# Kernel optimization log

Hardware: AMD Instinct MI355X
Metric: run time of the kernel (lower is better)

## Reference

```python
import jax, jax.numpy as jnp
import numpy as np

N_NODES = 50000
N_EDGES = 1500000
D = 512
LN_EPS = 1e-5


def setup_inputs() -> dict:
    key = jax.random.key(0)
    ks = jax.random.split(key, 8)
    scale = 1.0 / np.sqrt(D)
    return {
        "node_feature": jax.random.normal(ks[0], (N_NODES, D), dtype=jnp.float32),
        "edge_index": jax.random.randint(ks[1], (2, N_EDGES), 0, N_NODES, dtype=jnp.int32),
        "W_l": jax.random.uniform(ks[2], (D, D), jnp.float32, -scale, scale),  # neighbor lin
        "b_l": jnp.zeros((D,), jnp.float32),
        "W_r": jax.random.uniform(ks[3], (D, D), jnp.float32, -scale, scale),  # root lin (no bias)
        "gamma": jnp.ones((D,), jnp.float32),
        "beta": jnp.zeros((D,), jnp.float32),
    }


def _layer_norm(x, gamma, beta):
    mu = jnp.mean(x, axis=-1, keepdims=True)
    var = jnp.mean(jnp.square(x - mu), axis=-1, keepdims=True)
    return (x - mu) * jax.lax.rsqrt(var + LN_EPS) * gamma + beta


def reference(node_feature, edge_index, W_l, b_l, W_r, gamma, beta):
    n = node_feature.shape[0]
    residual = node_feature
    h = _layer_norm(node_feature, gamma, beta)
    src, dst = edge_index[0], edge_index[1]
    # mean-aggregate source features at destinations (gather + segment scatter)
    summed = jax.ops.segment_sum(h[src], dst, num_segments=n)  # [N, D]
    cnt = jax.ops.segment_sum(jnp.ones((src.shape[0],), h.dtype), dst, num_segments=n)
    mean = summed / jnp.maximum(cnt, 1.0)[:, None]
    # SAGEConv: lin_l(aggregated) + lin_r(root); bias on lin_l
    out = mean @ W_l.T + b_l + h @ W_r.T
    out = jax.nn.relu(out)
    return out + residual
```

## Files before the change

### kernel.cpp

```cpp
#include <hip/hip_runtime.h>


#define D_DIM 512

typedef __bf16 bf16x8 __attribute__((ext_vector_type(8)));
typedef float f32x4 __attribute__((ext_vector_type(4)));
typedef float f32x2 __attribute__((ext_vector_type(2)));

__device__ __forceinline__ unsigned short f2bf(float f) {
  unsigned u = __float_as_uint(f);
  u += 0x7fffu + ((u >> 16) & 1u);
  return (unsigned short)(u >> 16);
}
__device__ __forceinline__ float bflo(unsigned u) { return __uint_as_float(u << 16); }
__device__ __forceinline__ float bfhi(unsigned u) { return __uint_as_float(u & 0xffff0000u); }
__device__ __forceinline__ unsigned packbf2(float lo, float hi) {
  return (unsigned)f2bf(lo) | ((unsigned)f2bf(hi) << 16);
}

__global__ void ln_kernel(const float* __restrict__ x, const float* __restrict__ gamma,
                          const float* __restrict__ beta, unsigned short* __restrict__ Acat,
                          unsigned char* __restrict__ h8, int n, int use_fp8) {
  int lane = threadIdx.x & 63;
  int row = blockIdx.x * 4 + (threadIdx.x >> 6);
  if (row >= n) return;
  const float* xr = x + (size_t)row * D_DIM + lane * 8;
  float4 a = *(const float4*)xr;
  float4 b = *(const float4*)(xr + 4);
  float sum = a.x + a.y + a.z + a.w + b.x + b.y + b.z + b.w;
  float sq = a.x * a.x + a.y * a.y + a.z * a.z + a.w * a.w +
             b.x * b.x + b.y * b.y + b.z * b.z + b.w * b.w;
#pragma unroll
  for (int m = 1; m < 64; m <<= 1) {
    sum += __shfl_xor(sum, m, 64);
    sq  += __shfl_xor(sq, m, 64);
  }
  float mu = sum * (1.0f / D_DIM);
  float var = sq * (1.0f / D_DIM) - mu * mu;
  float rs = rsqrtf(var + 1e-5f);
  const float* gp = gamma + lane * 8;
  const float* bp = beta + lane * 8;
  float4 g0 = *(const float4*)gp, g1 = *(const float4*)(gp + 4);
  float4 e0 = *(const float4*)bp, e1 = *(const float4*)(bp + 4);
  float h0 = (a.x - mu) * rs * g0.x + e0.x;
  float h1 = (a.y - mu) * rs * g0.y + e0.y;
  float h2 = (a.z - mu) * rs * g0.z + e0.z;
  float h3 = (a.w - mu) * rs * g0.w + e0.w;
  float h4 = (b.x - mu) * rs * g1.x + e1.x;
  float h5 = (b.y - mu) * rs * g1.y + e1.y;
  float h6 = (b.z - mu) * rs * g1.z + e1.z;
  float h7 = (b.w - mu) * rs * g1.w + e1.w;
  uint4 st = { packbf2(h0, h1), packbf2(h2, h3), packbf2(h4, h5), packbf2(h6, h7) };
  *(uint4*)(Acat + (size_t)row * 1024 + 512 + lane * 8) = st;
  if (use_fp8) {
    int p0 = __builtin_amdgcn_cvt_pk_fp8_f32(h0, h1, 0, false);
    p0 = __builtin_amdgcn_cvt_pk_fp8_f32(h2, h3, p0, true);
    int p1 = __builtin_amdgcn_cvt_pk_fp8_f32(h4, h5, 0, false);
    p1 = __builtin_amdgcn_cvt_pk_fp8_f32(h6, h7, p1, true);
    uint2 st2 = { (unsigned)p0, (unsigned)p1 };
    *(uint2*)(h8 + (size_t)row * 512 + lane * 8) = st2;
  }
}

__global__ void wconv_kernel(const float* __restrict__ Wl, const float* __restrict__ Wr,
                             unsigned short* __restrict__ Wcat) {
  int id = blockIdx.x * 256 + threadIdx.x;
  int j = id >> 9, k = id & 511;
  Wcat[(size_t)j * 1024 + k] = f2bf(Wl[id]);
  Wcat[(size_t)j * 1024 + 512 + k] = f2bf(Wr[id]);
}

__global__ void zero_kernel(int* __restrict__ p, int n) {
  int i = blockIdx.x * 256 + threadIdx.x;
  if (i < n) p[i] = 0;
}

__global__ void hist_kernel(const int* __restrict__ dst, int nE, int* __restrict__ cnt) {
  int e = blockIdx.x * 256 + threadIdx.x;
  if (e < nE) atomicAdd(&cnt[dst[e]], 1);
}

__global__ void scan1_kernel(const int* __restrict__ cnt, int n,
                             int* __restrict__ excl, int* __restrict__ bsums) {
  __shared__ int wsum[16];
  int gid = blockIdx.x * 1024 + threadIdx.x;
  int lane = threadIdx.x & 63, wave = threadIdx.x >> 6;
  int v = (gid < n) ? cnt[gid] : 0;
  int s = v;
#pragma unroll
  for (int d = 1; d < 64; d <<= 1) {
    int t = __shfl_up(s, d, 64);
    if (lane >= d) s += t;
  }
  if (lane == 63) wsum[wave] = s;
  __syncthreads();
  if (wave == 0) {
    int ws = (lane < 16) ? wsum[lane] : 0;
#pragma unroll
    for (int d = 1; d < 16; d <<= 1) {
      int t = __shfl_up(ws, d, 64);
      if (lane >= d) ws += t;
    }
    if (lane < 16) wsum[lane] = ws;
  }
  __syncthreads();
  int incl = s + ((wave > 0) ? wsum[wave - 1] : 0);
  if (gid < n) excl[gid] = incl - v;
  if (threadIdx.x == 1023) bsums[blockIdx.x] = incl;
}

__global__ void scan2_kernel(int* __restrict__ bsums, int nb) {
  int lane = threadIdx.x;
  int v = (lane < nb) ? bsums[lane] : 0;
  int s = v;
#pragma unroll
  for (int d = 1; d < 64; d <<= 1) {
    int t = __shfl_up(s, d, 64);
    if (lane >= d) s += t;
  }
  if (lane < nb) bsums[lane] = s - v;
}

__global__ void scan3_kernel(int* __restrict__ rowst, int* __restrict__ cur,
                             const int* __restrict__ bsums, int n, int nE) {
  int gid = blockIdx.x * 1024 + threadIdx.x;
  if (gid < n) {
    int r = rowst[gid] + bsums[blockIdx.x];
    rowst[gid] = r;
    cur[gid] = r;
  }
  if (gid == 0) rowst[n] = nE;
}

__global__ void scatter_kernel(const int* __restrict__ src, const int* __restrict__ dst,
                               int nE, int* __restrict__ cur, int* __restrict__ sorted_src) {
  int e = blockIdx.x * 256 + threadIdx.x;
  if (e < nE) {
    int p = atomicAdd(&cur[dst[e]], 1);
    sorted_src[p] = src[e];
  }
}

__device__ __forceinline__ void acc_bf(float* acc, uint4 r) {
  acc[0] += bflo(r.x); acc[1] += bfhi(r.x);
  acc[2] += bflo(r.y); acc[3] += bfhi(r.y);
  acc[4] += bflo(r.z); acc[5] += bfhi(r.z);
  acc[6] += bflo(r.w); acc[7] += bfhi(r.w);
}

__device__ __forceinline__ void acc_f8(float* acc, uint2 r) {
  f32x2 a = __builtin_amdgcn_cvt_pk_f32_fp8(r.x, false);
  f32x2 b = __builtin_amdgcn_cvt_pk_f32_fp8(r.x, true);
  f32x2 c = __builtin_amdgcn_cvt_pk_f32_fp8(r.y, false);
  f32x2 d = __builtin_amdgcn_cvt_pk_f32_fp8(r.y, true);
  acc[0] += a.x; acc[1] += a.y; acc[2] += b.x; acc[3] += b.y;
  acc[4] += c.x; acc[5] += c.y; acc[6] += d.x; acc[7] += d.y;
}

__global__ void agg_kernel(unsigned short* __restrict__ Acat,
                           const unsigned char* __restrict__ h8,
                           const int* __restrict__ rowst,
                           const int* __restrict__ sorted_src, int n, int use_fp8) {
  int lane = threadIdx.x & 63;
  int node = blockIdx.x * 4 + (threadIdx.x >> 6);
  if (node >= n) return;
  int s0 = rowst[node], s1 = rowst[node + 1];
  float acc[8] = {0.f, 0.f, 0.f, 0.f, 0.f, 0.f, 0.f, 0.f};
  if (use_fp8) {
    const unsigned char* hb = h8 + lane * 8;
    int e = s0;
    for (; e + 3 < s1; e += 4) {
      int i0 = sorted_src[e], i1 = sorted_src[e + 1];
      int i2 = sorted_src[e + 2], i3 = sorted_src[e + 3];
      uint2 r0 = *(const uint2*)(hb + (size_t)i0 * 512);
      uint2 r1 = *(const uint2*)(hb + (size_t)i1 * 512);
      uint2 r2 = *(const uint2*)(hb + (size_t)i2 * 512);
      uint2 r3 = *(const uint2*)(hb + (size_t)i3 * 512);
      acc_f8(acc, r0); acc_f8(acc, r1); acc_f8(acc, r2); acc_f8(acc, r3);
    }
    for (; e < s1; ++e) {
      uint2 r0 = *(const uint2*)(hb + (size_t)sorted_src[e] * 512);
      acc_f8(acc, r0);
    }
  } else {
    const unsigned short* hbase = Acat + 512 + lane * 8;
    int e = s0;
    for (; e + 3 < s1; e += 4) {
      int i0 = sorted_src[e], i1 = sorted_src[e + 1];
      int i2 = sorted_src[e + 2], i3 = sorted_src[e + 3];
      uint4 r0 = *(const uint4*)(hbase + (size_t)i0 * 1024);
      uint4 r1 = *(const uint4*)(hbase + (size_t)i1 * 1024);
      uint4 r2 = *(const uint4*)(hbase + (size_t)i2 * 1024);
      uint4 r3 = *(const uint4*)(hbase + (size_t)i3 * 1024);
      acc_bf(acc, r0); acc_bf(acc, r1); acc_bf(acc, r2); acc_bf(acc, r3);
    }
    for (; e < s1; ++e) {
      uint4 r0 = *(const uint4*)(hbase + (size_t)sorted_src[e] * 1024);
      acc_bf(acc, r0);
    }
  }
  int deg = s1 - s0;
  float sc = (deg > 0) ? (1.0f / (float)deg) : 0.0f;
  uint4 st = { packbf2(acc[0] * sc, acc[1] * sc), packbf2(acc[2] * sc, acc[3] * sc),
               packbf2(acc[4] * sc, acc[5] * sc), packbf2(acc[6] * sc, acc[7] * sc) };
  *(uint4*)(Acat + (size_t)node * 1024 + lane * 8) = st;
}

__device__ __forceinline__ void async16(const unsigned short* g, char* lds) {
  __builtin_amdgcn_global_load_lds((const __attribute__((address_space(1))) void*)g,
                                   (__attribute__((address_space(3))) void*)lds, 16, 0, 0);
}

__global__ __launch_bounds__(256) void gemm_kernel(
    const unsigned short* __restrict__ A,
    const unsigned short* __restrict__ B,
    const float* __restrict__ bias,
    const float* __restrict__ residual,
    float* __restrict__ out, int M, int Mblocks) {
  __shared__ unsigned short sA[2][4096];
  __shared__ unsigned short sB[2][4096];
  const int K = 1024;
  int t = threadIdx.x;
  int lane = t & 63, wave = t >> 6;
  int quad = lane >> 4, l16 = lane & 15;
  int b = blockIdx.x;
  int mb = (b >> 5) * 8 + (b & 7);
  int nb = (b >> 3) & 3;
  if (mb >= Mblocks) return;
  int mBase = mb * 128, nBase = nb * 128;
  int wm = (wave & 1) * 64, wn = (wave >> 1) * 64;

  const unsigned short* gA = A + (size_t)(mBase + (t >> 2)) * K + (t & 3) * 8;
  const unsigned short* gB = B + (size_t)(nBase + (t >> 2)) * K + (t & 3) * 8;

  f32x4 acc[4][4] = {};

  auto issue = [&](int ks, int buf) {
    char* a0 = (char*)&sA[buf][0] + wave * 1024;
    char* b0 = (char*)&sB[buf][0] + wave * 1024;
    async16(gA + ks, a0);
    async16(gA + (size_t)64 * K + ks, a0 + 4096);
    async16(gB + ks, b0);
    async16(gB + (size_t)64 * K + ks, b0 + 4096);
  };
  auto compute = [&](int buf) {
    const unsigned short* pA = &sA[buf][0];
    const unsigned short* pB = &sB[buf][0];
    bf16x8 af[4], bfr[4];
#pragma unroll
    for (int i = 0; i < 4; ++i)
      af[i] = *(const bf16x8*)(pA + (wm + i * 16 + l16) * 32 + quad * 8);
#pragma unroll
    for (int j = 0; j < 4; ++j)
      bfr[j] = *(const bf16x8*)(pB + (wn + j * 16 + l16) * 32 + quad * 8);
#pragma unroll
    for (int i = 0; i < 4; ++i)
#pragma unroll
      for (int j = 0; j < 4; ++j)
        acc[i][j] = __builtin_amdgcn_mfma_f32_16x16x32_bf16(af[i], bfr[j], acc[i][j], 0, 0, 0);
  };

  issue(0, 0);
  for (int r = 0; r < 31; ++r) {
    int cur = r & 1;
    issue((r + 1) << 5, cur ^ 1);
    asm volatile("s_waitcnt vmcnt(4)\n\ts_barrier" ::: "memory");
    compute(cur);
    asm volatile("s_barrier" ::: "memory");
  }
  asm volatile("s_waitcnt vmcnt(0)\n\ts_barrier" ::: "memory");
  compute(1);

  float biasv[4];
#pragma unroll
  for (int j = 0; j < 4; ++j) biasv[j] = bias[nBase + wn + j * 16 + l16];
#pragma unroll
  for (int i = 0; i < 4; ++i) {
    int gr0 = mBase + wm + i * 16 + quad * 4;
#pragma unroll
    for (int j = 0; j < 4; ++j) {
      int col = nBase + wn + j * 16 + l16;
#pragma unroll
      for (int r = 0; r < 4; ++r) {
        int gr = gr0 + r;
        if (gr < M) {
          size_t idx = (size_t)gr * D_DIM + col;
          float v = acc[i][j][r] + biasv[j];
          float rv = __builtin_nontemporal_load(&residual[idx]);
          __builtin_nontemporal_store(fmaxf(v, 0.0f) + rv, &out[idx]);
        }
      }
    }
  }
}

extern "C" void kernel_launch(void* const* d_in, const int* in_sizes, int n_in,
                              void* d_out, int out_size, void* d_ws, size_t ws_size,
                              hipStream_t stream) {
  const float* x = (const float*)d_in[0];
  const int* ei = (const int*)d_in[1];
  const float* Wl = (const float*)d_in[2];
  const float* bl = (const float*)d_in[3];
  const float* Wr = (const float*)d_in[4];
  const float* gamma = (const float*)d_in[5];
  const float* beta = (const float*)d_in[6];
  float* out = (float*)d_out;

  int n = in_sizes[0] / D_DIM;
  int nE = in_sizes[1] / 2;
  const int* src = ei;
  const int* dstv = ei + nE;
  int Mpad = (n + 127) & ~127;
  int Mblocks = Mpad / 128;

  char* w = (char*)d_ws;
  size_t off = 0;
  auto carve = [&](size_t bytes) {
    char* p = w + off;
    off += (bytes + 255) & ~(size_t)255;
    return p;
  };
  unsigned short* Acat = (unsigned short*)carve((size_t)Mpad * 1024 * 2);
  unsigned short* Wcat = (unsigned short*)carve((size_t)512 * 1024 * 2);
  int* sorted = (int*)carve((size_t)nE * 4);
  int* cnt = (int*)carve((size_t)n * 4);
  int* rowst = (int*)carve((size_t)(n + 1) * 4);
  int* bsums = (int*)carve(1024);
  if (off > ws_size) return;

  size_t h8_bytes = (size_t)n * 512;
  int use_fp8 = (off + h8_bytes <= ws_size) ? 1 : 0;
  unsigned char* h8 = use_fp8 ? (unsigned char*)carve(h8_bytes) : (unsigned char*)w;

  int nbScan = (n + 1023) / 1024;

  ln_kernel<<<(n + 3) / 4, 256, 0, stream>>>(x, gamma, beta, Acat, h8, n, use_fp8);
  wconv_kernel<<<(512 * 512) / 256, 256, 0, stream>>>(Wl, Wr, Wcat);
  zero_kernel<<<(n + 255) / 256, 256, 0, stream>>>(cnt, n);
  hist_kernel<<<(nE + 255) / 256, 256, 0, stream>>>(dstv, nE, cnt);
  scan1_kernel<<<nbScan, 1024, 0, stream>>>(cnt, n, rowst, bsums);
  scan2_kernel<<<1, 64, 0, stream>>>(bsums, nbScan);
  scan3_kernel<<<nbScan, 1024, 0, stream>>>(rowst, cnt, bsums, n, nE);
  scatter_kernel<<<(nE + 255) / 256, 256, 0, stream>>>(src, dstv, nE, cnt, sorted);
  agg_kernel<<<(n + 3) / 4, 256, 0, stream>>>(Acat, h8, rowst, sorted, n, use_fp8);
  int gemmBlocks = ((Mblocks + 7) / 8) * 32;
  gemm_kernel<<<gemmBlocks, 256, 0, stream>>>(Acat, Wcat, bl, x, out, n, Mblocks);
}
```

Baseline: 647.6 us.

## Load GEMM fragments directly from global memory into registers, dropping LDS staging

The GEMM no longer stages A/B tiles through LDS with async global-to-LDS loads and barriers. Each wave now loads its MFMA fragments straight from global memory into registers, double-buffered across K steps. The MFMA operands are swapped so each lane's accumulator holds four consecutive output columns, which lets the epilogue use 16-byte vector loads and stores for bias, residual and output. The cost is that tile data is no longer shared between waves in LDS, so more redundant global/L2 traffic is issued, with uncoalesced 16-byte row fragments.

```diff
diff --git a/kernel.cpp b/kernel.cpp
--- a/kernel.cpp
+++ b/kernel.cpp
@@ -206,19 +206,12 @@
   *(uint4*)(Acat + (size_t)node * 1024 + lane * 8) = st;
 }
 
-__device__ __forceinline__ void async16(const unsigned short* g, char* lds) {
-  __builtin_amdgcn_global_load_lds((const __attribute__((address_space(1))) void*)g,
-                                   (__attribute__((address_space(3))) void*)lds, 16, 0, 0);
-}
-
 __global__ __launch_bounds__(256) void gemm_kernel(
-    const unsigned short* __restrict__ A,
-    const unsigned short* __restrict__ B,
+    const unsigned short* __restrict__ X,
+    const unsigned short* __restrict__ W,
     const float* __restrict__ bias,
     const float* __restrict__ residual,
     float* __restrict__ out, int M, int Mblocks) {
-  __shared__ unsigned short sA[2][4096];
-  __shared__ unsigned short sB[2][4096];
   const int K = 1024;
   int t = threadIdx.x;
   int lane = t & 63, wave = t >> 6;
@@ -227,68 +220,57 @@
   int mb = (b >> 5) * 8 + (b & 7);
   int nb = (b >> 3) & 3;
   if (mb >= Mblocks) return;
-  int mBase = mb * 128, nBase = nb * 128;
-  int wm = (wave & 1) * 64, wn = (wave >> 1) * 64;
-
-  const unsigned short* gA = A + (size_t)(mBase + (t >> 2)) * K + (t & 3) * 8;
-  const unsigned short* gB = B + (size_t)(nBase + (t >> 2)) * K + (t & 3) * 8;
-
+  int rowBase = mb * 128 + (wave & 1) * 64;
+  int colBase = nb * 128 + (wave >> 1) * 64;
+
+  const unsigned short* pX = X + (size_t)(rowBase + l16) * K + quad * 8;
+  const unsigned short* pW = W + (size_t)(colBase + l16) * K + quad * 8;
+
+  bf16x8 xf0[4], wf0[4], xf1[4], wf1[4];
   f32x4 acc[4][4] = {};
 
-  auto issue = [&](int ks, int buf) {
-    char* a0 = (char*)&sA[buf][0] + wave * 1024;
-    char* b0 = (char*)&sB[buf][0] + wave * 1024;
-    async16(gA + ks, a0);
-    async16(gA + (size_t)64 * K + ks, a0 + 4096);
-    async16(gB + ks, b0);
-    async16(gB + (size_t)64 * K + ks, b0 + 4096);
+  auto loadf = [&](int ks, bf16x8* xf, bf16x8* wf) {
+#pragma unroll
+    for (int j = 0; j < 4; ++j)
+      xf[j] = *(const bf16x8*)(pX + (size_t)(j * 16) * K + ks);
+#pragma unroll
+    for (int i = 0; i < 4; ++i)
+      wf[i] = *(const bf16x8*)(pW + (size_t)(i * 16) * K + ks);
   };
-  auto compute = [&](int buf) {
-    const unsigned short* pA = &sA[buf][0];
-    const unsigned short* pB = &sB[buf][0];
-    bf16x8 af[4], bfr[4];
+  auto domfma = [&](bf16x8* xf, bf16x8* wf) {
 #pragma unroll
     for (int i = 0; i < 4; ++i)
-      af[i] = *(const bf16x8*)(pA + (wm + i * 16 + l16) * 32 + quad * 8);
-#pragma unroll
-    for (int j = 0; j < 4; ++j)
-      bfr[j] = *(const bf16x8*)(pB + (wn + j * 16 + l16) * 32 + quad * 8);
-#pragma unroll
-    for (int i = 0; i < 4; ++i)
 #pragma unroll
       for (int j = 0; j < 4; ++j)
-        acc[i][j] = __builtin_amdgcn_mfma_f32_16x16x32_bf16(af[i], bfr[j], acc[i][j], 0, 0, 0);
+        acc[i][j] = __builtin_amdgcn_mfma_f32_16x16x32_bf16(wf[i], xf[j], acc[i][j], 0, 0, 0);
   };
 
-  issue(0, 0);
-  for (int r = 0; r < 31; ++r) {
-    int cur = r & 1;
-    issue((r + 1) << 5, cur ^ 1);
-    asm volatile("s_waitcnt vmcnt(4)\n\ts_barrier" ::: "memory");
-    compute(cur);
-    asm volatile("s_barrier" ::: "memory");
-  }
-  asm volatile("s_waitcnt vmcnt(0)\n\ts_barrier" ::: "memory");
-  compute(1);
-
-  float biasv[4];
-#pragma unroll
-  for (int j = 0; j < 4; ++j) biasv[j] = bias[nBase + wn + j * 16 + l16];
-#pragma unroll
-  for (int i = 0; i < 4; ++i) {
-    int gr0 = mBase + wm + i * 16 + quad * 4;
-#pragma unroll
-    for (int j = 0; j < 4; ++j) {
-      int col = nBase + wn + j * 16 + l16;
-#pragma unroll
-      for (int r = 0; r < 4; ++r) {
-        int gr = gr0 + r;
-        if (gr < M) {
-          size_t idx = (size_t)gr * D_DIM + col;
-          float v = acc[i][j][r] + biasv[j];
-          float rv = __builtin_nontemporal_load(&residual[idx]);
-          __builtin_nontemporal_store(fmaxf(v, 0.0f) + rv, &out[idx]);
-        }
+  loadf(0, xf0, wf0);
+#pragma unroll 1
+  for (int it = 0; it < 16; ++it) {
+    loadf(it * 64 + 32, xf1, wf1);
+    domfma(xf0, wf0);
+    loadf((it * 64 + 64) & (K - 1), xf0, wf0);
+    domfma(xf1, wf1);
+  }
+
+  f32x4 bv[4];
+#pragma unroll
+  for (int i = 0; i < 4; ++i)
+    bv[i] = *(const f32x4*)(bias + colBase + i * 16 + quad * 4);
+#pragma unroll
+  for (int j = 0; j < 4; ++j) {
+    int row = rowBase + j * 16 + l16;
+    if (row < M) {
+#pragma unroll
+      for (int i = 0; i < 4; ++i) {
+        size_t idx = (size_t)row * D_DIM + colBase + i * 16 + quad * 4;
+        f32x4 rv = __builtin_nontemporal_load((const f32x4*)(residual + idx));
+        f32x4 o;
+#pragma unroll
+        for (int r = 0; r < 4; ++r)
+          o[r] = fmaxf(acc[i][j][r] + bv[i][r], 0.0f) + rv[r];
+        __builtin_nontemporal_store(o, (f32x4*)(out + idx));
       }
     }
   }
```

Measured after the change: 690.9 us. +6.7%, slower.
